# Kernel optimization log

Hardware: AMD Instinct MI355X
Metric: run time of the kernel (lower is better)

## Reference

```python
import jax, jax.numpy as jnp
import numpy as np

D_MODEL = 1024
D_HIDDEN = 2048
BATCH = 2
SEQ = 4096


def setup_inputs() -> dict:
    key = jax.random.key(0)
    ks = jax.random.split(key, 14)
    d, h = D_MODEL, D_HIDDEN
    s_d = 1.0 / np.sqrt(d)
    s_h = 1.0 / np.sqrt(h)
    x = jax.random.normal(ks[0], (BATCH, SEQ, d), jnp.float32)
    W1 = jax.random.normal(ks[1], (d, d), jnp.float32) * s_d
    W2 = jax.random.normal(ks[2], (d, d), jnp.float32) * s_d
    Wlast = jax.random.normal(ks[3], (d, d), jnp.float32) * s_d
    conv_w = jax.random.normal(ks[4], (d, 1, 3), jnp.float32) * 0.5  # depthwise (O, I/g=1, K)
    conv_b = jnp.zeros((d,), jnp.float32)
    A = jax.random.normal(ks[5], (h,), jnp.float32)
    Wb = jax.random.normal(ks[6], (h, d), jnp.float32) * s_d
    bb = jnp.zeros((h,), jnp.float32)
    Wc = jax.random.normal(ks[7], (d, h), jnp.float32) * s_h
    bc = jnp.zeros((d,), jnp.float32)
    Wd = jax.random.normal(ks[8], (d, d), jnp.float32) * s_d
    bd = jnp.zeros((d,), jnp.float32)
    # small delta so cumsum(delta*A) over SEQ steps stays O(1) (avoids exp overflow)
    Wdelta = jax.random.normal(ks[9], (h, d), jnp.float32) * 0.01
    bdelta = jnp.full((h,), -8.0, jnp.float32)
    return dict(x=x, W1=W1, conv_w=conv_w, conv_b=conv_b, A=A, Wb=Wb, bb=bb,
                Wc=Wc, bc=bc, Wd=Wd, bd=bd, Wdelta=Wdelta, bdelta=bdelta,
                W2=W2, Wlast=Wlast)


def reference(x, W1, conv_w, conv_b, A, Wb, bb, Wc, bc, Wd, bd, Wdelta, bdelta, W2, Wlast):
    # x: [B, L, d]
    x1 = x @ W1.T  # linear1 (no bias)
    # depthwise conv1d, kernel 3, pad 1, groups = d_model
    xc = jax.lax.conv_general_dilated(
        x1.transpose(0, 2, 1), conv_w,
        window_strides=(1,), padding=[(1, 1)],
        feature_group_count=D_MODEL,
        dimension_numbers=('NCH', 'OIH', 'NCH')) + conv_b[None, :, None]
    xa = jax.nn.silu(xc.transpose(0, 2, 1))  # [B, L, d]
    # SSM: delta/A/B discretization + cumprod-cumsum scan along sequence
    delta = jax.nn.softplus(xa @ Wdelta.T + bdelta)  # [B, L, h]
    A_bar = jnp.exp(delta * A)
    B_bar = delta * (xa @ Wb.T + bb)
    A_cum = jnp.cumprod(A_bar, axis=1)
    h_st = jnp.cumsum(B_bar / A_cum, axis=1) * A_cum  # [B, L, h]
    out_ssm = (h_st @ Wc.T + bc) + (xa @ Wd.T + bd)  # [B, L, d]
    # gated residual
    x_res = jax.nn.silu(out_ssm @ W2.T)
    z = out_ssm * x_res
    return out_ssm + z @ Wlast.T
```

## Files before the change

kernel.cpp:

```cpp
#include <hip/hip_runtime.h>
#include <cstdint>
#include <cstddef>

#define DMODEL 1024
#define DH 2048
#define BATCH 2
#define SEQ 4096
#define MROWS (BATCH*SEQ)
#define CHUNK 64
#define NCHUNK (SEQ/CHUNK)

typedef unsigned short u16;
typedef __attribute__((ext_vector_type(8))) short bf16x8;
typedef __attribute__((ext_vector_type(4))) float f32x4;

__device__ __forceinline__ u16 f2bf(float f) {
    union { float f; unsigned u; } v; v.f = f;
    unsigned r = v.u + 0x7FFFu + ((v.u >> 16) & 1u);
    return (u16)(r >> 16);
}
__device__ __forceinline__ float bf2f(u16 h) {
    union { unsigned u; float f; } v; v.u = ((unsigned)h) << 16; return v.f;
}

__device__ __forceinline__ float softplus_fast(float x) {
    if (x < -4.f) return __expf(x);
    return (x > 0.f) ? (x + log1pf(__expf(-x))) : log1pf(__expf(x));
}
__device__ __forceinline__ float silu_fast(float v) {
    return v * __fdividef(1.f, 1.f + __expf(-v));
}

__global__ void cvt_bf16(const float* __restrict__ src, u16* __restrict__ dst, int n4) {
    int i = blockIdx.x * blockDim.x + threadIdx.x;
    if (i >= n4) return;
    const float4 v = reinterpret_cast<const float4*>(src)[i];
    ushort4 o;
    o.x = f2bf(v.x); o.y = f2bf(v.y); o.z = f2bf(v.z); o.w = f2bf(v.w);
    reinterpret_cast<ushort4*>(dst)[i] = o;
}

__device__ __forceinline__ void gload_lds16(const void* g, void* l) {
    __builtin_amdgcn_global_load_lds(
        (const __attribute__((address_space(1))) void*)g,
        (__attribute__((address_space(3))) void*)l,
        16, 0, 0);
}

template<int EP, bool TWOK>
__global__ __launch_bounds__(256) void gemm_bt(
    const u16* __restrict__ A1, const u16* __restrict__ B1, int K1,
    const u16* __restrict__ A2, const u16* __restrict__ B2, int K2,
    float* __restrict__ C, u16* __restrict__ Cb, u16* __restrict__ Cb2,
    const float* __restrict__ bias, const float* __restrict__ bias2,
    const float* __restrict__ aux,
    int M, int N)
{
    __shared__ u16 As[128*64];
    __shared__ u16 Bs[128*64];
    const int tid = threadIdx.x;

    const int nwg = gridDim.x * gridDim.y;
    int wg = blockIdx.y * gridDim.x + blockIdx.x;
    wg = (wg & 7) * (nwg >> 3) + (wg >> 3);
    const int m0 = (wg / gridDim.x) * 128;
    const int n0 = (wg % gridDim.x) * 128;

    const int wave = tid >> 6, lane = tid & 63;
    const int wr = (wave >> 1) * 64;
    const int wc = (wave & 1) * 64;
    const int fr = lane & 15, fq = lane >> 4;

    f32x4 acc[4][4];
    #pragma unroll
    for (int m = 0; m < 4; m++)
        #pragma unroll
        for (int n = 0; n < 4; n++) acc[m][n] = f32x4{0.f, 0.f, 0.f, 0.f};

    const int nseg = TWOK ? 2 : 1;
    for (int seg = 0; seg < nseg; ++seg) {
        const u16* A = (TWOK && seg) ? A2 : A1;
        const u16* B = (TWOK && seg) ? B2 : B1;
        const int  K = (TWOK && seg) ? K2 : K1;
        for (int k0 = 0; k0 < K; k0 += 64) {
            #pragma unroll
            for (int i = 0; i < 4; ++i) {
                const int g = i*256 + tid;
                const int r = g >> 3;
                const int ch = (g & 7) ^ (r & 7);
                gload_lds16(A + (size_t)(m0 + r)*K + (k0 + ch*8), (char*)As + (size_t)g*16);
                gload_lds16(B + (size_t)(n0 + r)*K + (k0 + ch*8), (char*)Bs + (size_t)g*16);
            }
            __syncthreads();
            #pragma unroll
            for (int kk = 0; kk < 2; ++kk) {
                bf16x8 af[4], bfr[4];
                #pragma unroll
                for (int m = 0; m < 4; m++) {
                    const int r = wr + m*16 + fr;
                    af[m] = *reinterpret_cast<const bf16x8*>(
                        (const char*)As + r*128 + (((kk*4 + fq) ^ (r & 7)) * 16));
                }
                #pragma unroll
                for (int n = 0; n < 4; n++) {
                    const int r = wc + n*16 + fr;
                    bfr[n] = *reinterpret_cast<const bf16x8*>(
                        (const char*)Bs + r*128 + (((kk*4 + fq) ^ (r & 7)) * 16));
                }
                #pragma unroll
                for (int m = 0; m < 4; m++)
                    #pragma unroll
                    for (int n = 0; n < 4; n++)
                        acc[m][n] = __builtin_amdgcn_mfma_f32_16x16x32_bf16(af[m], bfr[n], acc[m][n], 0, 0, 0);
            }
            __syncthreads();
        }
    }

    #pragma unroll
    for (int m = 0; m < 4; m++) {
        #pragma unroll
        for (int n = 0; n < 4; n++) {
            const int col = n0 + wc + n*16 + fr;
            float bv = 0.f;
            if constexpr (EP != 4) {
                if (bias)  bv += bias[col];
                if (bias2) bv += bias2[col];
            }
            #pragma unroll
            for (int j = 0; j < 4; j++) {
                const int row = m0 + wr + m*16 + fq*4 + j;
                const size_t idx = (size_t)row * N + col;
                float v = acc[m][n][j] + bv;
                if constexpr (EP == 0) {
                    Cb[idx] = f2bf(v);
                } else if constexpr (EP == 1) {
                    C[idx] = v;
                    Cb[idx] = f2bf(v);
                } else if constexpr (EP == 2) {
                    Cb[idx] = f2bf(aux[idx] * silu_fast(v));
                } else if constexpr (EP == 3) {
                    C[idx] = aux[idx] + v;
                } else {
                    if (col < DH) {
                        Cb [(size_t)row*DH + col]        = f2bf(softplus_fast(v + bias[col]));
                    } else {
                        Cb2[(size_t)row*DH + (col - DH)] = f2bf(v + bias2[col - DH]);
                    }
                }
            }
        }
    }
}

__global__ void conv_silu8(const u16* __restrict__ x1, const float* __restrict__ cw,
                           const float* __restrict__ cb, u16* __restrict__ xab) {
    int t = blockIdx.x * blockDim.x + threadIdx.x;
    int c8  = t & (DMODEL/8 - 1);
    int row = t >> 7;
    int l = row & (SEQ - 1);
    const int c0 = c8 * 8;
    const size_t i0 = (size_t)row * DMODEL + c0;
    bf16x8 v0 = *reinterpret_cast<const bf16x8*>(x1 + i0);
    bf16x8 vm = {}; if (l > 0)       vm = *reinterpret_cast<const bf16x8*>(x1 + i0 - DMODEL);
    bf16x8 vp = {}; if (l < SEQ - 1) vp = *reinterpret_cast<const bf16x8*>(x1 + i0 + DMODEL);
    if (l == 0)       vm = bf16x8{};
    if (l == SEQ - 1) vp = bf16x8{};
    bf16x8 o;
    #pragma unroll
    for (int j = 0; j < 8; ++j) {
        const int c = c0 + j;
        float v = cw[c*3+0]*bf2f((u16)vm[j]) + cw[c*3+1]*bf2f((u16)v0[j])
                + cw[c*3+2]*bf2f((u16)vp[j]) + cb[c];
        o[j] = (short)f2bf(silu_fast(v));
    }
    *reinterpret_cast<bf16x8*>(xab + i0) = o;
}

__global__ void scan_chunks(const u16* __restrict__ delta, const u16* __restrict__ pBv,
                            const float* __restrict__ Avec,
                            float* __restrict__ cA, float* __restrict__ cB) {
    const int c = blockIdx.x * blockDim.x + threadIdx.x;
    const int q = blockIdx.y;
    const int b = blockIdx.z;
    const float Ac = Avec[c];
    float hA = 1.f, hB = 0.f;
    size_t base = ((size_t)b*SEQ + q*CHUNK)*DH + c;
    for (int j = 0; j < CHUNK; ++j) {
        float d = bf2f(delta[base]);
        float Abar = __expf(d * Ac);
        hA *= Abar;
        hB = Abar*hB + d * bf2f(pBv[base]);
        base += DH;
    }
    size_t o = ((size_t)b*NCHUNK + q)*DH + c;
    cA[o] = hA; cB[o] = hB;
}

__global__ void scan_prefix(const float* __restrict__ cA, const float* __restrict__ cB,
                            float* __restrict__ cH) {
    const int t = blockIdx.x * blockDim.x + threadIdx.x;
    const int b = t >> 11;
    const int c = t & (DH - 1);
    float h = 0.f;
    size_t o = ((size_t)b*NCHUNK)*DH + c;
    float a = cA[o], bb = cB[o];
    for (int q = 0; q < NCHUNK; ++q) {
        const size_t on = o + DH;
        float a2 = 0.f, b2 = 0.f;
        if (q + 1 < NCHUNK) { a2 = cA[on]; b2 = cB[on]; }
        cH[o] = h;
        h = a*h + bb;
        a = a2; bb = b2; o = on;
    }
}

__global__ void scan_apply(const u16* __restrict__ delta, const u16* __restrict__ pBv,
                           const float* __restrict__ Avec, const float* __restrict__ cH,
                           u16* __restrict__ hstb) {
    const int c = blockIdx.x * blockDim.x + threadIdx.x;
    const int q = blockIdx.y;
    const int b = blockIdx.z;
    const float Ac = Avec[c];
    float h = cH[((size_t)b*NCHUNK + q)*DH + c];
    size_t base = ((size_t)b*SEQ + q*CHUNK)*DH + c;
    for (int j = 0; j < CHUNK; ++j) {
        float d = bf2f(delta[base]);
        float Abar = __expf(d * Ac);
        h = Abar*h + d * bf2f(pBv[base]);
        hstb[base] = f2bf(h);
        base += DH;
    }
}

extern "C" void kernel_launch(void* const* d_in, const int* in_sizes, int n_in,
                              void* d_out, int out_size, void* d_ws, size_t ws_size,
                              hipStream_t stream) {
    const float* x      = (const float*)d_in[0];
    const float* W1     = (const float*)d_in[1];
    const float* conv_w = (const float*)d_in[2];
    const float* conv_b = (const float*)d_in[3];
    const float* Avec   = (const float*)d_in[4];
    const float* Wb     = (const float*)d_in[5];
    const float* bb     = (const float*)d_in[6];
    const float* Wc     = (const float*)d_in[7];
    const float* bc     = (const float*)d_in[8];
    const float* Wd     = (const float*)d_in[9];
    const float* bd     = (const float*)d_in[10];
    const float* Wdelta = (const float*)d_in[11];
    const float* bdelta = (const float*)d_in[12];
    const float* W2     = (const float*)d_in[13];
    const float* Wlast  = (const float*)d_in[14];
    float* out = (float*)d_out;
    (void)in_sizes; (void)n_in; (void)out_size;

    struct Ptrs {
        u16 *sW;
        float *cA, *cB, *cH;
        u16 *xb, *x1b, *xab, *delta, *pBv, *ossb, *hstb, *zb;
        float *oss;
        size_t total;
    };
    auto layout = [&](int passes) -> Ptrs {
        Ptrs P{};
        const size_t Mp = MROWS / passes;
        const int nb = BATCH / passes;
        size_t off = 0;
        auto al = [&](size_t bytes) -> char* {
            char* p = (char*)d_ws + off; off += (bytes + 255) & ~(size_t)255; return p;
        };
        P.sW  = (u16*)al((size_t)2*DH*DMODEL*2);
        P.cA  = (float*)al((size_t)nb*NCHUNK*DH*4);
        P.cB  = (float*)al((size_t)nb*NCHUNK*DH*4);
        P.cH  = (float*)al((size_t)nb*NCHUNK*DH*4);
        char* RA = al(Mp*DMODEL*2);
        char* RB = al(Mp*DMODEL*2);
        char* RC = al(Mp*DMODEL*2);
        char* RD = al(Mp*DH*2);
        char* RE = al(Mp*DH*2);
        char* RF = al(Mp*DH*2);
        P.xb    = (u16*)RA; P.ossb = (u16*)RA;
        P.x1b   = (u16*)RB; P.zb   = (u16*)RB;
        P.xab   = (u16*)RC;
        P.delta = (u16*)RD; P.oss  = (float*)RD;
        P.pBv   = (u16*)RE;
        P.hstb  = (u16*)RF;
        P.total = off;
        return P;
    };

    int passes = (ws_size >= layout(1).total) ? 1 : 2;
    Ptrs P = layout(passes);
    if (ws_size < P.total) return;
    const int Mp = MROWS / passes;
    const int nb = BATCH / passes;

    const dim3 blk(256);
    auto cvt = [&](const float* s, u16* d, size_t n) {
        int n4 = (int)(n / 4);
        cvt_bf16<<<dim3((n4 + 255)/256), blk, 0, stream>>>(s, d, n4);
    };
    const dim3 gD (DMODEL/128,   Mp/128);
    const dim3 gDB(2*DH/128,     Mp/128);
    u16* sW2 = P.sW + (size_t)DH*DMODEL;

    for (int p = 0; p < passes; ++p) {
        const float* x_p  = x  + (size_t)p*Mp*DMODEL;
        float*      out_p = out + (size_t)p*Mp*DMODEL;

        cvt(x_p, P.xb, (size_t)Mp*DMODEL);
        cvt(W1, P.sW, (size_t)DMODEL*DMODEL);
        gemm_bt<0,false><<<gD, blk, 0, stream>>>(P.xb, P.sW, DMODEL, nullptr, nullptr, 0,
                                                 nullptr, P.x1b, nullptr, nullptr, nullptr, nullptr, Mp, DMODEL);
        conv_silu8<<<dim3(Mp*DMODEL/8/256), blk, 0, stream>>>(P.x1b, conv_w, conv_b, P.xab);
        cvt(Wdelta, P.sW, (size_t)DH*DMODEL);
        cvt(Wb,     sW2,  (size_t)DH*DMODEL);
        gemm_bt<4,false><<<gDB, blk, 0, stream>>>(P.xab, P.sW, DMODEL, nullptr, nullptr, 0,
                                                  nullptr, P.delta, P.pBv, bdelta, bb, nullptr, Mp, 2*DH);
        scan_chunks<<<dim3(DH/256, NCHUNK, nb), blk, 0, stream>>>(P.delta, P.pBv, Avec, P.cA, P.cB);
        scan_prefix<<<dim3(nb*DH/256), blk, 0, stream>>>(P.cA, P.cB, P.cH);
        scan_apply <<<dim3(DH/256, NCHUNK, nb), blk, 0, stream>>>(P.delta, P.pBv, Avec, P.cH, P.hstb);
        cvt(Wd, P.sW, (size_t)DMODEL*DMODEL);
        cvt(Wc, sW2,  (size_t)DMODEL*DH);
        gemm_bt<1,true><<<gD, blk, 0, stream>>>(P.xab, P.sW, DMODEL, P.hstb, sW2, DH,
                                                P.oss, P.ossb, nullptr, bd, bc, nullptr, Mp, DMODEL);
        cvt(W2, P.sW, (size_t)DMODEL*DMODEL);
        gemm_bt<2,false><<<gD, blk, 0, stream>>>(P.ossb, P.sW, DMODEL, nullptr, nullptr, 0,
                                                 nullptr, P.zb, nullptr, nullptr, nullptr, P.oss, Mp, DMODEL);
        cvt(Wlast, P.sW, (size_t)DMODEL*DMODEL);
        gemm_bt<3,false><<<gD, blk, 0, stream>>>(P.zb, P.sW, DMODEL, nullptr, nullptr, 0,
                                                 out_p, nullptr, nullptr, nullptr, nullptr, P.oss, Mp, DMODEL);
    }
}
```

Baseline: 370.1 us.

## Double-buffer LDS tiles to overlap global loads with MFMA compute

The GEMM kernel now uses two LDS buffers for the A and B tiles. It issues the next K-tile's global-to-LDS loads before computing on the current tile, so load latency is hidden behind the MFMA work. The two K segments are merged into one flattened tile loop. This doubles LDS use to 64KB per block, which may lower occupancy, and it relies on an explicit vmcnt wait plus a barrier per iteration.

```diff
diff --git a/kernel.cpp b/kernel.cpp
--- a/kernel.cpp
+++ b/kernel.cpp
@@ -56,8 +56,8 @@
     const float* __restrict__ aux,
     int M, int N)
 {
-    __shared__ u16 As[128*64];
-    __shared__ u16 Bs[128*64];
+    __shared__ u16 As[2][128*64];
+    __shared__ u16 Bs[2][128*64];
     const int tid = threadIdx.x;
 
     const int nwg = gridDim.x * gridDim.y;
@@ -77,44 +77,59 @@
         #pragma unroll
         for (int n = 0; n < 4; n++) acc[m][n] = f32x4{0.f, 0.f, 0.f, 0.f};
 
-    const int nseg = TWOK ? 2 : 1;
-    for (int seg = 0; seg < nseg; ++seg) {
-        const u16* A = (TWOK && seg) ? A2 : A1;
-        const u16* B = (TWOK && seg) ? B2 : B1;
-        const int  K = (TWOK && seg) ? K2 : K1;
-        for (int k0 = 0; k0 < K; k0 += 64) {
+    const int nt1 = K1 >> 6;
+    const int nt  = TWOK ? nt1 + (K2 >> 6) : nt1;
+
+    auto stage = [&](int t, int buf) {
+        const u16* A = A1; const u16* B = B1; int K = K1; int k0 = t << 6;
+        if (TWOK && t >= nt1) { A = A2; B = B2; K = K2; k0 = (t - nt1) << 6; }
+        #pragma unroll
+        for (int i = 0; i < 4; ++i) {
+            const int g = i*256 + tid;
+            const int r = g >> 3;
+            const int ch = (g & 7) ^ (r & 7);
+            gload_lds16(A + (size_t)(m0 + r)*K + (k0 + ch*8), (char*)As[buf] + (size_t)g*16);
+            gload_lds16(B + (size_t)(n0 + r)*K + (k0 + ch*8), (char*)Bs[buf] + (size_t)g*16);
+        }
+    };
+
+    auto compute = [&](int buf) {
+        #pragma unroll
+        for (int kk = 0; kk < 2; ++kk) {
+            bf16x8 af[4], bfr[4];
             #pragma unroll
-            for (int i = 0; i < 4; ++i) {
-                const int g = i*256 + tid;
-                const int r = g >> 3;
-                const int ch = (g & 7) ^ (r & 7);
-                gload_lds16(A + (size_t)(m0 + r)*K + (k0 + ch*8), (char*)As + (size_t)g*16);
-                gload_lds16(B + (size_t)(n0 + r)*K + (k0 + ch*8), (char*)Bs + (size_t)g*16);
+            for (int m = 0; m < 4; m++) {
+                const int r = wr + m*16 + fr;
+                af[m] = *reinterpret_cast<const bf16x8*>(
+                    (const char*)As[buf] + r*128 + (((kk*4 + fq) ^ (r & 7)) * 16));
             }
-            __syncthreads();
             #pragma unroll
-            for (int kk = 0; kk < 2; ++kk) {
-                bf16x8 af[4], bfr[4];
+            for (int n = 0; n < 4; n++) {
+                const int r = wc + n*16 + fr;
+                bfr[n] = *reinterpret_cast<const bf16x8*>(
+                    (const char*)Bs[buf] + r*128 + (((kk*4 + fq) ^ (r & 7)) * 16));
+            }
+            #pragma unroll
+            for (int m = 0; m < 4; m++)
                 #pragma unroll
-                for (int m = 0; m < 4; m++) {
-                    const int r = wr + m*16 + fr;
-                    af[m] = *reinterpret_cast<const bf16x8*>(
-                        (const char*)As + r*128 + (((kk*4 + fq) ^ (r & 7)) * 16));
-                }
-                #pragma unroll
-                for (int n = 0; n < 4; n++) {
-                    const int r = wc + n*16 + fr;
-                    bfr[n] = *reinterpret_cast<const bf16x8*>(
-                        (const char*)Bs + r*128 + (((kk*4 + fq) ^ (r & 7)) * 16));
-                }
-                #pragma unroll
-                for (int m = 0; m < 4; m++)
-                    #pragma unroll
-                    for (int n = 0; n < 4; n++)
-                        acc[m][n] = __builtin_amdgcn_mfma_f32_16x16x32_bf16(af[m], bfr[n], acc[m][n], 0, 0, 0);
-            }
-            __syncthreads();
+                for (int n = 0; n < 4; n++)
+                    acc[m][n] = __builtin_amdgcn_mfma_f32_16x16x32_bf16(af[m], bfr[n], acc[m][n], 0, 0, 0);
         }
+    };
+
+    stage(0, 0);
+    asm volatile("s_waitcnt vmcnt(0)" ::: "memory");
+    __builtin_amdgcn_s_barrier();
+    __builtin_amdgcn_sched_barrier(0);
+
+    int cur = 0;
+    for (int t = 0; t < nt; ++t) {
+        if (t + 1 < nt) stage(t + 1, cur ^ 1);
+        compute(cur);
+        asm volatile("s_waitcnt vmcnt(0)" ::: "memory");
+        __builtin_amdgcn_s_barrier();
+        __builtin_amdgcn_sched_barrier(0);
+        cur ^= 1;
     }
 
     #pragma unroll
```

Result: faster. 352.7 us (-4.7%).

## Enlarge GEMM tile to 256x128 with 8 waves and supertile swizzle

Applied to the files above, without the earlier changes.

The GEMM kernel now uses 512 threads and a 256x128 output tile. The A tile in LDS doubles to 256 rows while B stays at 128 rows, so each B fetch is reused across more rows, and the two-segment K loop is flattened into one loop. Workgroups are remapped into 8x8 supertiles to improve L2 locality. The costs are a grid half as large, more LDS per block and possibly lower occupancy. The hidden epilogue still indexes rows via wr = (wave>>1)*64, which with 8 waves spans 256 rows, so it appears consistent.

```diff
diff --git a/kernel.cpp b/kernel.cpp
--- a/kernel.cpp
+++ b/kernel.cpp
@@ -48,7 +48,7 @@
 }
 
 template<int EP, bool TWOK>
-__global__ __launch_bounds__(256) void gemm_bt(
+__global__ __launch_bounds__(512) void gemm_bt(
     const u16* __restrict__ A1, const u16* __restrict__ B1, int K1,
     const u16* __restrict__ A2, const u16* __restrict__ B2, int K2,
     float* __restrict__ C, u16* __restrict__ Cb, u16* __restrict__ Cb2,
@@ -56,15 +56,20 @@
     const float* __restrict__ aux,
     int M, int N)
 {
-    __shared__ u16 As[128*64];
+    __shared__ u16 As[256*64];
     __shared__ u16 Bs[128*64];
     const int tid = threadIdx.x;
 
     const int nwg = gridDim.x * gridDim.y;
     int wg = blockIdx.y * gridDim.x + blockIdx.x;
     wg = (wg & 7) * (nwg >> 3) + (wg >> 3);
-    const int m0 = (wg / gridDim.x) * 128;
-    const int n0 = (wg % gridDim.x) * 128;
+    const int stile = wg >> 6;
+    const int t64   = wg & 63;
+    const int nSn   = gridDim.x >> 3;
+    const int sm = (nSn > 0) ? stile / nSn : stile;
+    const int sn = (nSn > 0) ? stile - sm * nSn : 0;
+    const int m0 = (sm * 8 + (t64 >> 3)) * 256;
+    const int n0 = (sn * 8 + (t64 & 7)) * 128;
 
     const int wave = tid >> 6, lane = tid & 63;
     const int wr = (wave >> 1) * 64;
@@ -77,44 +82,50 @@
         #pragma unroll
         for (int n = 0; n < 4; n++) acc[m][n] = f32x4{0.f, 0.f, 0.f, 0.f};
 
-    const int nseg = TWOK ? 2 : 1;
-    for (int seg = 0; seg < nseg; ++seg) {
-        const u16* A = (TWOK && seg) ? A2 : A1;
-        const u16* B = (TWOK && seg) ? B2 : B1;
-        const int  K = (TWOK && seg) ? K2 : K1;
-        for (int k0 = 0; k0 < K; k0 += 64) {
+    const int nt1 = K1 >> 6;
+    const int nt  = TWOK ? nt1 + (K2 >> 6) : nt1;
+
+    for (int t = 0; t < nt; ++t) {
+        const u16* A = A1; const u16* B = B1; int K = K1; int k0 = t << 6;
+        if (TWOK && t >= nt1) { A = A2; B = B2; K = K2; k0 = (t - nt1) << 6; }
+        #pragma unroll
+        for (int i = 0; i < 4; ++i) {
+            const int g = i*512 + tid;
+            const int r = g >> 3;
+            const int ch = (g & 7) ^ (r & 7);
+            gload_lds16(A + (size_t)(m0 + r)*K + (k0 + ch*8), (char*)As + (size_t)g*16);
+        }
+        #pragma unroll
+        for (int i = 0; i < 2; ++i) {
+            const int g = i*512 + tid;
+            const int r = g >> 3;
+            const int ch = (g & 7) ^ (r & 7);
+            gload_lds16(B + (size_t)(n0 + r)*K + (k0 + ch*8), (char*)Bs + (size_t)g*16);
+        }
+        __syncthreads();
+
+        #pragma unroll
+        for (int kk = 0; kk < 2; ++kk) {
+            bf16x8 af[4], bfr[4];
             #pragma unroll
-            for (int i = 0; i < 4; ++i) {
-                const int g = i*256 + tid;
-                const int r = g >> 3;
-                const int ch = (g & 7) ^ (r & 7);
-                gload_lds16(A + (size_t)(m0 + r)*K + (k0 + ch*8), (char*)As + (size_t)g*16);
-                gload_lds16(B + (size_t)(n0 + r)*K + (k0 + ch*8), (char*)Bs + (size_t)g*16);
+            for (int m = 0; m < 4; m++) {
+                const int r = wr + m*16 + fr;
+                af[m] = *reinterpret_cast<const bf16x8*>(
+                    (const char*)As + r*128 + (((kk*4 + fq) ^ (r & 7)) * 16));
             }
-            __syncthreads();
             #pragma unroll
-            for (int kk = 0; kk < 2; ++kk) {
-                bf16x8 af[4], bfr[4];
+            for (int n = 0; n < 4; n++) {
+                const int r = wc + n*16 + fr;
+                bfr[n] = *reinterpret_cast<const bf16x8*>(
+                    (const char*)Bs + r*128 + (((kk*4 + fq) ^ (r & 7)) * 16));
+            }
+            #pragma unroll
+            for (int m = 0; m < 4; m++)
                 #pragma unroll
-                for (int m = 0; m < 4; m++) {
-                    const int r = wr + m*16 + fr;
-                    af[m] = *reinterpret_cast<const bf16x8*>(
-                        (const char*)As + r*128 + (((kk*4 + fq) ^ (r & 7)) * 16));
-                }
-                #pragma unroll
-                for (int n = 0; n < 4; n++) {
-                    const int r = wc + n*16 + fr;
-                    bfr[n] = *reinterpret_cast<const bf16x8*>(
-                        (const char*)Bs + r*128 + (((kk*4 + fq) ^ (r & 7)) * 16));
-                }
-                #pragma unroll
-                for (int m = 0; m < 4; m++)
-                    #pragma unroll
-                    for (int n = 0; n < 4; n++)
-                        acc[m][n] = __builtin_amdgcn_mfma_f32_16x16x32_bf16(af[m], bfr[n], acc[m][n], 0, 0, 0);
-            }
-            __syncthreads();
+                for (int n = 0; n < 4; n++)
+                    acc[m][n] = __builtin_amdgcn_mfma_f32_16x16x32_bf16(af[m], bfr[n], acc[m][n], 0, 0, 0);
         }
+        __syncthreads();
     }
 
     #pragma unroll
@@ -296,12 +307,13 @@
     const int nb = BATCH / passes;
 
     const dim3 blk(256);
+    const dim3 blkG(512);
     auto cvt = [&](const float* s, u16* d, size_t n) {
         int n4 = (int)(n / 4);
         cvt_bf16<<<dim3((n4 + 255)/256), blk, 0, stream>>>(s, d, n4);
     };
-    const dim3 gD (DMODEL/128,   Mp/128);
-    const dim3 gDB(2*DH/128,     Mp/128);
+    const dim3 gD (DMODEL/128, Mp/256);
+    const dim3 gDB(2*DH/128,   Mp/256);
     u16* sW2 = P.sW + (size_t)DH*DMODEL;
 
     for (int p = 0; p < passes; ++p) {
@@ -310,25 +322,25 @@
 
         cvt(x_p, P.xb, (size_t)Mp*DMODEL);
         cvt(W1, P.sW, (size_t)DMODEL*DMODEL);
-        gemm_bt<0,false><<<gD, blk, 0, stream>>>(P.xb, P.sW, DMODEL, nullptr, nullptr, 0,
+        gemm_bt<0,false><<<gD, blkG, 0, stream>>>(P.xb, P.sW, DMODEL, nullptr, nullptr, 0,
                                                  nullptr, P.x1b, nullptr, nullptr, nullptr, nullptr, Mp, DMODEL);
         conv_silu8<<<dim3(Mp*DMODEL/8/256), blk, 0, stream>>>(P.x1b, conv_w, conv_b, P.xab);
         cvt(Wdelta, P.sW, (size_t)DH*DMODEL);
         cvt(Wb,     sW2,  (size_t)DH*DMODEL);
-        gemm_bt<4,false><<<gDB, blk, 0, stream>>>(P.xab, P.sW, DMODEL, nullptr, nullptr, 0,
+        gemm_bt<4,false><<<gDB, blkG, 0, stream>>>(P.xab, P.sW, DMODEL, nullptr, nullptr, 0,
                                                   nullptr, P.delta, P.pBv, bdelta, bb, nullptr, Mp, 2*DH);
         scan_chunks<<<dim3(DH/256, NCHUNK, nb), blk, 0, stream>>>(P.delta, P.pBv, Avec, P.cA, P.cB);
         scan_prefix<<<dim3(nb*DH/256), blk, 0, stream>>>(P.cA, P.cB, P.cH);
         scan_apply <<<dim3(DH/256, NCHUNK, nb), blk, 0, stream>>>(P.delta, P.pBv, Avec, P.cH, P.hstb);
         cvt(Wd, P.sW, (size_t)DMODEL*DMODEL);
         cvt(Wc, sW2,  (size_t)DMODEL*DH);
-        gemm_bt<1,true><<<gD, blk, 0, stream>>>(P.xab, P.sW, DMODEL, P.hstb, sW2, DH,
+        gemm_bt<1,true><<<gD, blkG, 0, stream>>>(P.xab, P.sW, DMODEL, P.hstb, sW2, DH,
                                                 P.oss, P.ossb, nullptr, bd, bc, nullptr, Mp, DMODEL);
         cvt(W2, P.sW, (size_t)DMODEL*DMODEL);
-        gemm_bt<2,false><<<gD, blk, 0, stream>>>(P.ossb, P.sW, DMODEL, nullptr, nullptr, 0,
+        gemm_bt<2,false><<<gD, blkG, 0, stream>>>(P.ossb, P.sW, DMODEL, nullptr, nullptr, 0,
                                                  nullptr, P.zb, nullptr, nullptr, nullptr, P.oss, Mp, DMODEL);
         cvt(Wlast, P.sW, (size_t)DMODEL*DMODEL);
-        gemm_bt<3,false><<<gD, blk, 0, stream>>>(P.zb, P.sW, DMODEL, nullptr, nullptr, 0,
+        gemm_bt<3,false><<<gD, blkG, 0, stream>>>(P.zb, P.sW, DMODEL, nullptr, nullptr, 0,
                                                  out_p, nullptr, nullptr, nullptr, nullptr, P.oss, Mp, DMODEL);
     }
 }
```

New measurement: 360.0 us. -2.7%, faster.

## Double GEMM K-tile to 128, remap tiles into 8x8 supertiles, stage epilogue through LDS

Applied to the files above, without the earlier changes.

The GEMM kernel now loads 128-wide K slices (64KB LDS) instead of 64-wide ones, which halves the number of barrier pairs per K loop. Workgroups are remapped so that groups of 64 form 8x8 tile blocks for better L2 reuse of the A and B panels. The epilogue writes accumulators to LDS in two half-tile passes, then emits coalesced vectorized float4/ushort4 stores with vector bias loads. The larger LDS footprint limits occupancy to fewer workgroups per CU and adds extra barriers in the epilogue.

```diff
diff --git a/kernel.cpp b/kernel.cpp
--- a/kernel.cpp
+++ b/kernel.cpp
@@ -56,15 +56,23 @@
     const float* __restrict__ aux,
     int M, int N)
 {
-    __shared__ u16 As[128*64];
-    __shared__ u16 Bs[128*64];
+    __shared__ __align__(16) char smem[65536];
+    u16* As = (u16*)smem;
+    u16* Bs = (u16*)(smem + 32768);
+    float* ep = (float*)smem;
+
     const int tid = threadIdx.x;
 
     const int nwg = gridDim.x * gridDim.y;
     int wg = blockIdx.y * gridDim.x + blockIdx.x;
     wg = (wg & 7) * (nwg >> 3) + (wg >> 3);
-    const int m0 = (wg / gridDim.x) * 128;
-    const int n0 = (wg % gridDim.x) * 128;
+    const int stile = wg >> 6;
+    const int t64   = wg & 63;
+    const int nSn   = gridDim.x >> 3;
+    const int sm = (nSn > 0) ? stile / nSn : stile;
+    const int sn = (nSn > 0) ? stile - sm * nSn : 0;
+    const int m0 = (sm * 8 + (t64 >> 3)) * 128;
+    const int n0 = (sn * 8 + (t64 & 7)) * 128;
 
     const int wave = tid >> 6, lane = tid & 63;
     const int wr = (wave >> 1) * 64;
@@ -77,79 +85,119 @@
         #pragma unroll
         for (int n = 0; n < 4; n++) acc[m][n] = f32x4{0.f, 0.f, 0.f, 0.f};
 
-    const int nseg = TWOK ? 2 : 1;
-    for (int seg = 0; seg < nseg; ++seg) {
-        const u16* A = (TWOK && seg) ? A2 : A1;
-        const u16* B = (TWOK && seg) ? B2 : B1;
-        const int  K = (TWOK && seg) ? K2 : K1;
-        for (int k0 = 0; k0 < K; k0 += 64) {
+    const int nt1 = K1 >> 7;
+    const int nt  = TWOK ? nt1 + (K2 >> 7) : nt1;
+
+    for (int t = 0; t < nt; ++t) {
+        const u16* A = A1; const u16* B = B1; int K = K1; int k0 = t << 7;
+        if (TWOK && t >= nt1) { A = A2; B = B2; K = K2; k0 = (t - nt1) << 7; }
+        #pragma unroll
+        for (int i = 0; i < 8; ++i) {
+            const int g = i*256 + tid;
+            const int r = g >> 4;
+            const int ch = (g & 15) ^ (r & 15);
+            gload_lds16(A + (size_t)(m0 + r)*K + (k0 + ch*8), (char*)As + (size_t)g*16);
+        }
+        #pragma unroll
+        for (int i = 0; i < 8; ++i) {
+            const int g = i*256 + tid;
+            const int r = g >> 4;
+            const int ch = (g & 15) ^ (r & 15);
+            gload_lds16(B + (size_t)(n0 + r)*K + (k0 + ch*8), (char*)Bs + (size_t)g*16);
+        }
+        __syncthreads();
+
+        #pragma unroll
+        for (int kk = 0; kk < 4; ++kk) {
+            bf16x8 af[4], bfr[4];
             #pragma unroll
-            for (int i = 0; i < 4; ++i) {
-                const int g = i*256 + tid;
-                const int r = g >> 3;
-                const int ch = (g & 7) ^ (r & 7);
-                gload_lds16(A + (size_t)(m0 + r)*K + (k0 + ch*8), (char*)As + (size_t)g*16);
-                gload_lds16(B + (size_t)(n0 + r)*K + (k0 + ch*8), (char*)Bs + (size_t)g*16);
+            for (int m = 0; m < 4; m++) {
+                const int r = wr + m*16 + fr;
+                af[m] = *reinterpret_cast<const bf16x8*>(
+                    (const char*)As + r*256 + (((kk*4 + fq) ^ (r & 15)) * 16));
             }
-            __syncthreads();
             #pragma unroll
-            for (int kk = 0; kk < 2; ++kk) {
-                bf16x8 af[4], bfr[4];
+            for (int n = 0; n < 4; n++) {
+                const int r = wc + n*16 + fr;
+                bfr[n] = *reinterpret_cast<const bf16x8*>(
+                    (const char*)Bs + r*256 + (((kk*4 + fq) ^ (r & 15)) * 16));
+            }
+            #pragma unroll
+            for (int m = 0; m < 4; m++)
                 #pragma unroll
-                for (int m = 0; m < 4; m++) {
-                    const int r = wr + m*16 + fr;
-                    af[m] = *reinterpret_cast<const bf16x8*>(
-                        (const char*)As + r*128 + (((kk*4 + fq) ^ (r & 7)) * 16));
-                }
+                for (int n = 0; n < 4; n++)
+                    acc[m][n] = __builtin_amdgcn_mfma_f32_16x16x32_bf16(af[m], bfr[n], acc[m][n], 0, 0, 0);
+        }
+        __syncthreads();
+    }
+
+    const bool isDelta = (EP == 4) ? (n0 < DH) : false;
+    #pragma unroll
+    for (int c = 0; c < 2; ++c) {
+        if ((wave >> 1) == c) {
+            #pragma unroll
+            for (int m = 0; m < 4; m++)
                 #pragma unroll
                 for (int n = 0; n < 4; n++) {
-                    const int r = wc + n*16 + fr;
-                    bfr[n] = *reinterpret_cast<const bf16x8*>(
-                        (const char*)Bs + r*128 + (((kk*4 + fq) ^ (r & 7)) * 16));
-                }
-                #pragma unroll
-                for (int m = 0; m < 4; m++)
+                    const int col = wc + n*16 + fr;
                     #pragma unroll
-                    for (int n = 0; n < 4; n++)
-                        acc[m][n] = __builtin_amdgcn_mfma_f32_16x16x32_bf16(af[m], bfr[n], acc[m][n], 0, 0, 0);
+                    for (int j = 0; j < 4; j++)
+                        ep[(m*16 + fq*4 + j)*132 + col] = acc[m][n][j];
+                }
+        }
+        __syncthreads();
+        #pragma unroll
+        for (int p = 0; p < 8; ++p) {
+            const int idx = p*256 + tid;
+            const int row = idx >> 5, c4 = idx & 31;
+            float4 v = *reinterpret_cast<const float4*>(&ep[row*132 + c4*4]);
+            const int rg   = m0 + c*64 + row;
+            const int colg = n0 + c4*4;
+            if constexpr (EP == 4) {
+                const int cc = isDelta ? colg : (colg - DH);
+                const float4 bv = *reinterpret_cast<const float4*>(
+                    (isDelta ? bias : bias2) + cc);
+                ushort4 o;
+                if (isDelta) {
+                    o.x = f2bf(softplus_fast(v.x + bv.x));
+                    o.y = f2bf(softplus_fast(v.y + bv.y));
+                    o.z = f2bf(softplus_fast(v.z + bv.z));
+                    o.w = f2bf(softplus_fast(v.w + bv.w));
+                } else {
+                    o.x = f2bf(v.x + bv.x); o.y = f2bf(v.y + bv.y);
+                    o.z = f2bf(v.z + bv.z); o.w = f2bf(v.w + bv.w);
+                }
+                *reinterpret_cast<ushort4*>((isDelta ? Cb : Cb2) + (size_t)rg*DH + cc) = o;
+            } else {
+                if (bias) {
+                    const float4 b1 = *reinterpret_cast<const float4*>(bias + colg);
+                    v.x += b1.x; v.y += b1.y; v.z += b1.z; v.w += b1.w;
+                }
+                if (bias2) {
+                    const float4 b2 = *reinterpret_cast<const float4*>(bias2 + colg);
+                    v.x += b2.x; v.y += b2.y; v.z += b2.z; v.w += b2.w;
+                }
+                const size_t gidx = (size_t)rg * N + colg;
+                if constexpr (EP == 0) {
+                    ushort4 o = { f2bf(v.x), f2bf(v.y), f2bf(v.z), f2bf(v.w) };
+                    *reinterpret_cast<ushort4*>(Cb + gidx) = o;
+                } else if constexpr (EP == 1) {
+                    *reinterpret_cast<float4*>(C + gidx) = v;
+                    ushort4 o = { f2bf(v.x), f2bf(v.y), f2bf(v.z), f2bf(v.w) };
+                    *reinterpret_cast<ushort4*>(Cb + gidx) = o;
+                } else if constexpr (EP == 2) {
+                    const float4 a = *reinterpret_cast<const float4*>(aux + gidx);
+                    ushort4 o = { f2bf(a.x * silu_fast(v.x)), f2bf(a.y * silu_fast(v.y)),
+                                  f2bf(a.z * silu_fast(v.z)), f2bf(a.w * silu_fast(v.w)) };
+                    *reinterpret_cast<ushort4*>(Cb + gidx) = o;
+                } else {
+                    const float4 a = *reinterpret_cast<const float4*>(aux + gidx);
+                    float4 o = { a.x + v.x, a.y + v.y, a.z + v.z, a.w + v.w };
+                    *reinterpret_cast<float4*>(C + gidx) = o;
+                }
             }
-            __syncthreads();
-        }
-    }
-
-    #pragma unroll
-    for (int m = 0; m < 4; m++) {
-        #pragma unroll
-        for (int n = 0; n < 4; n++) {
-            const int col = n0 + wc + n*16 + fr;
-            float bv = 0.f;
-            if constexpr (EP != 4) {
-                if (bias)  bv += bias[col];
-                if (bias2) bv += bias2[col];
-            }
-            #pragma unroll
-            for (int j = 0; j < 4; j++) {
-                const int row = m0 + wr + m*16 + fq*4 + j;
-                const size_t idx = (size_t)row * N + col;
-                float v = acc[m][n][j] + bv;
-                if constexpr (EP == 0) {
-                    Cb[idx] = f2bf(v);
-                } else if constexpr (EP == 1) {
-                    C[idx] = v;
-                    Cb[idx] = f2bf(v);
-                } else if constexpr (EP == 2) {
-                    Cb[idx] = f2bf(aux[idx] * silu_fast(v));
-                } else if constexpr (EP == 3) {
-                    C[idx] = aux[idx] + v;
-                } else {
-                    if (col < DH) {
-                        Cb [(size_t)row*DH + col]        = f2bf(softplus_fast(v + bias[col]));
-                    } else {
-                        Cb2[(size_t)row*DH + (col - DH)] = f2bf(v + bias2[col - DH]);
-                    }
-                }
-            }
-        }
+        }
+        __syncthreads();
     }
 }
 
@@ -300,8 +348,8 @@
         int n4 = (int)(n / 4);
         cvt_bf16<<<dim3((n4 + 255)/256), blk, 0, stream>>>(s, d, n4);
     };
-    const dim3 gD (DMODEL/128,   Mp/128);
-    const dim3 gDB(2*DH/128,     Mp/128);
+    const dim3 gD (DMODEL/128, Mp/128);
+    const dim3 gDB(2*DH/128,   Mp/128);
     u16* sW2 = P.sW + (size_t)DH*DMODEL;
 
     for (int p = 0; p < passes; ++p) {
```

Result: faster. 321.1 us (-13.2%).
